# Kernel optimization log

Hardware: AMD Instinct MI355X
Metric: run time of the kernel (lower is better)

The kernel has to match this reference:

```python
import jax, jax.numpy as jnp
import numpy as np

# Llama-3-8B-like attention, prefill over B sequences of length S (flattened tokens)
D = 4096      # hidden_size
N = 32        # num query heads
K = 8         # num KV heads (GQA)
H = 128       # head_dim (== head_dim_original, already a multiple of 128 so no padding)
B = 4         # sequences in the ragged batch
S = 1024      # tokens per sequence
T = B * S     # total flattened tokens
ROPE_THETA = 10000.0


def _apply_rope(x, positions, head_dim, theta):
    # x: [T, n_heads, H]; positions: [T] int
    inv_freq = 1.0 / (theta ** (jnp.arange(0, head_dim, 2, dtype=jnp.float32) / head_dim))
    freqs = positions.astype(jnp.float32)[:, None] * inv_freq[None, :]  # [T, H/2]
    emb = jnp.concatenate([freqs, freqs], axis=-1)                       # [T, H]
    cos = jnp.cos(emb)[:, None, :].astype(x.dtype)
    sin = jnp.sin(emb)[:, None, :].astype(x.dtype)
    x1, x2 = jnp.split(x, 2, axis=-1)
    rotated = jnp.concatenate([-x2, x1], axis=-1)
    return x * cos + rotated * sin


def setup_inputs() -> dict:
    key = jax.random.key(0)
    ks = jax.random.split(key, 5)
    x = jax.random.normal(ks[0], (T, D), dtype=jnp.float32)
    # positions restart per sequence (ragged prefill metadata)
    input_positions = (jnp.arange(T, dtype=jnp.int32) % S)
    w_scale = 0.02
    Wq = jax.random.normal(ks[1], (D, N, H), dtype=jnp.float32) * w_scale
    Wk = jax.random.normal(ks[2], (D, K, H), dtype=jnp.float32) * w_scale
    Wv = jax.random.normal(ks[3], (D, K, H), dtype=jnp.float32) * w_scale
    Wo = jax.random.normal(ks[4], (N, H, D), dtype=jnp.float32) * w_scale
    return {"x": x, "input_positions": input_positions,
            "Wq": Wq, "Wk": Wk, "Wv": Wv, "Wo": Wo}


def reference(x, input_positions, Wq, Wk, Wv, Wo):
    # QKV projections (flattened tokens)
    q = jnp.einsum('td,dnh->tnh', x, Wq)   # [T, N, H]
    k = jnp.einsum('td,dkh->tkh', x, Wk)   # [T, K, H]
    v = jnp.einsum('td,dkh->tkh', x, Wv)   # [T, K, H]
    q = _apply_rope(q, input_positions, H, ROPE_THETA)
    k = _apply_rope(k, input_positions, H, ROPE_THETA)

    # Ragged causal attention: per-sequence causal SDPA with GQA head grouping.
    G = N // K  # query heads per KV head
    qb = q.reshape(B, S, K, G, H)
    kb = k.reshape(B, S, K, H)
    vb = v.reshape(B, S, K, H)
    scale = jnp.asarray(H, q.dtype) ** -0.5  # head_dim_original ** -0.5
    scores = jnp.einsum('bqkgh,bskh->bkgqs', qb, kb) * scale  # [B,K,G,S,S]
    causal = jnp.tril(jnp.ones((S, S), dtype=bool))
    scores = jnp.where(causal, scores, jnp.finfo(scores.dtype).min)
    probs = jax.nn.softmax(scores, axis=-1)
    out = jnp.einsum('bkgqs,bskh->bqkgh', probs, vb).reshape(T, N, H)

    # Output projection
    o = jnp.einsum('tnh,nhd->td', out, Wo)  # [T, D]
    return o
```

## Files before the change

kernel.cpp:

```cpp
#include <hip/hip_runtime.h>
#include <cstdint>


typedef unsigned short u16;
typedef short bf16x8 __attribute__((ext_vector_type(8)));
typedef float f32x4 __attribute__((ext_vector_type(4)));

#define L2E 1.44269504088896340736f

static __device__ __forceinline__ u16 f2bf(float f) {
  union { float f; unsigned u; } v; v.f = f;
  unsigned r = (v.u + 0x7fffu + ((v.u >> 16) & 1u)) >> 16;
  return (u16)r;
}
static __device__ __forceinline__ float bf2f(u16 h) {
  union { unsigned u; float f; } v; v.u = ((unsigned)h) << 16;
  return v.f;
}

typedef __attribute__((address_space(1))) const unsigned int gas_u32;
typedef __attribute__((address_space(3))) unsigned int las_u32;
static __device__ __forceinline__ void glds16(const void* g, const void* l) {
  __builtin_amdgcn_global_load_lds((gas_u32*)(uintptr_t)g,
                                   (las_u32*)(unsigned)(uintptr_t)l, 16, 0, 0);
}

__global__ __launch_bounds__(256) void cvt_kernel(const float4* __restrict__ in,
                                                  uint2* __restrict__ out, int n4) {
  int i = blockIdx.x * 256 + threadIdx.x;
  if (i < n4) {
    float4 v = in[i];
    uint2 r;
    r.x = (unsigned)f2bf(v.x) | ((unsigned)f2bf(v.y) << 16);
    r.y = (unsigned)f2bf(v.z) | ((unsigned)f2bf(v.w) << 16);
    out[i] = r;
  }
}

__global__ __launch_bounds__(256) void tcvt_kernel(const float* __restrict__ in,
                                                   u16* __restrict__ out, int R, int C) {
  __shared__ float tile[32][33];
  int tx = threadIdx.x, ty = threadIdx.y;
  int r0 = blockIdx.y * 32, c0 = blockIdx.x * 32;
#pragma unroll
  for (int j = 0; j < 4; ++j)
    tile[ty + j * 8][tx] = in[(size_t)(r0 + ty + j * 8) * C + c0 + tx];
  __syncthreads();
#pragma unroll
  for (int j = 0; j < 4; ++j)
    out[(size_t)(c0 + ty + j * 8) * R + r0 + tx] = f2bf(tile[tx][ty + j * 8]);
}

template <int BF16OUT>
__global__ __launch_bounds__(256, 2) void gemm_nt(const u16* __restrict__ A,
                                                  const u16* __restrict__ Bm,
                                                  void* __restrict__ Cp,
                                                  int M, int N, int Kd) {
  __shared__ u16 Al[128 * 64];
  __shared__ u16 Bl[128 * 64];
  const int tid = threadIdx.x;
  const int w = tid >> 6, lane = tid & 63;
  const int ln15 = lane & 15, quad = lane >> 4;
  const int wm = w & 1, wn = w >> 1;
  const int m0 = blockIdx.y * 128, n0 = blockIdx.x * 128;

  const int rA = w * 8 + (lane >> 3);
  const int cA = (((lane & 7) ^ (rA & 7)) << 3);
  const u16* aptr = A + (size_t)(m0 + rA) * Kd + cA;
  const u16* bptr = Bm + (size_t)(n0 + rA) * Kd + cA;

  f32x4 acc[4][4];
#pragma unroll
  for (int i = 0; i < 4; ++i)
#pragma unroll
    for (int j = 0; j < 4; ++j) acc[i][j] = f32x4{0.f, 0.f, 0.f, 0.f};

  for (int k0 = 0; k0 < Kd; k0 += 64) {
    __syncthreads();
#pragma unroll
    for (int q = 0; q < 4; ++q) {
      glds16(aptr + (size_t)q * 32 * Kd, &Al[(q * 32 + w * 8) * 64]);
      glds16(bptr + (size_t)q * 32 * Kd, &Bl[(q * 32 + w * 8) * 64]);
    }
    aptr += 64; bptr += 64;
    __syncthreads();
#pragma unroll
    for (int ks = 0; ks < 2; ++ks) {
      bf16x8 af[4], bfr[4];
#pragma unroll
      for (int t = 0; t < 4; ++t) {
        int ra = wm * 64 + t * 16 + ln15;
        int pa = (ks * 4 + quad) ^ (ra & 7);
        af[t] = *(const bf16x8*)&Al[ra * 64 + pa * 8];
        int rb = wn * 64 + t * 16 + ln15;
        int pb = (ks * 4 + quad) ^ (rb & 7);
        bfr[t] = *(const bf16x8*)&Bl[rb * 64 + pb * 8];
      }
#pragma unroll
      for (int mt = 0; mt < 4; ++mt)
#pragma unroll
        for (int nt = 0; nt < 4; ++nt)
          acc[mt][nt] =
              __builtin_amdgcn_mfma_f32_16x16x32_bf16(af[mt], bfr[nt], acc[mt][nt], 0, 0, 0);
    }
  }

#pragma unroll
  for (int mt = 0; mt < 4; ++mt) {
#pragma unroll
    for (int nt = 0; nt < 4; ++nt) {
      int row = m0 + wm * 64 + mt * 16 + quad * 4;
      int col = n0 + wn * 64 + nt * 16 + ln15;
#pragma unroll
      for (int r = 0; r < 4; ++r) {
        float v = acc[mt][nt][r];
        if (BF16OUT)
          ((u16*)Cp)[(size_t)(row + r) * N + col] = f2bf(v);
        else
          ((float*)Cp)[(size_t)(row + r) * N + col] = v;
      }
    }
  }
}

__global__ __launch_bounds__(256) void rope_kernel(u16* __restrict__ qkv,
                                                   const int* __restrict__ pos, int total) {
  int idx = blockIdx.x * 256 + threadIdx.x;
  if (idx >= total) return;
  int t = idx / 2560;
  int rem = idx - t * 2560;
  int head = rem >> 6;
  int i = rem & 63;
  float p = (float)pos[t];
  float inv = exp2f(-0.20751874963942190927f * (float)i);
  float f = p * inv;
  float s, c;
  sincosf(f, &s, &c);
  int colbase = (head < 32) ? head * 128 : (4096 + (head - 32) * 128);
  u16* base = qkv + (size_t)t * 6144 + colbase;
  float x1 = bf2f(base[i]), x2 = bf2f(base[i + 64]);
  float o1 = x1 * c - x2 * s;
  float o2 = x2 * c + x1 * s;
  if (head < 32) { o1 *= 0.08838834764831845f; o2 *= 0.08838834764831845f; }
  base[i] = f2bf(o1);
  base[i + 64] = f2bf(o2);
}

__global__ __launch_bounds__(256, 3) void attn_kernel(const u16* __restrict__ qkv,
                                                      u16* __restrict__ outp) {
  __shared__ u16 Klds[64 * 128];
  __shared__ u16 Vtlds[128 * 72];
  __shared__ u16 Plds[4 * 16 * 72];

  const int bx = blockIdx.x;
  const int qb = 15 - (bx & 15);
  const int n = (bx >> 4) & 31;
  const int b = bx >> 9;
  const int kh = n >> 2;

  const int tid = threadIdx.x;
  const int w = tid >> 6;
  const int lane = tid & 63;
  const int ln15 = lane & 15;
  const int quad = lane >> 4;

  const int ldq = 6144;
  const int seq0 = b << 10;
  const int q0 = seq0 + qb * 64;

  const u16* Qg = qkv + n * 128;
  const u16* Kg = qkv + 4096 + kh * 128;
  const u16* Vg = qkv + 5120 + kh * 128;

  bf16x8 qf[4];
  {
    const u16* qrow = Qg + (size_t)(q0 + w * 16 + ln15) * ldq + quad * 8;
#pragma unroll
    for (int ks = 0; ks < 4; ++ks) qf[ks] = *(const bf16x8*)(qrow + ks * 32);
  }

  f32x4 o[8];
#pragma unroll
  for (int i = 0; i < 8; ++i) o[i] = f32x4{0.f, 0.f, 0.f, 0.f};
  float m_r[4] = {-INFINITY, -INFINITY, -INFINITY, -INFINITY};
  float l_r[4] = {0.f, 0.f, 0.f, 0.f};

  const int krow = w * 4 + (lane >> 4);
  const int kcol = (((lane & 15) ^ (krow & 7)) << 3);

  const int vs0 = (lane & 31) * 2;
  const int vhb = w * 32 + (lane >> 5) * 16;

  for (int kt = 0; kt <= qb; ++kt) {
    __syncthreads();
    {
      const u16* kbase = Kg + (size_t)(seq0 + kt * 64 + krow) * ldq + kcol;
#pragma unroll
      for (int q = 0; q < 4; ++q)
        glds16(kbase + (size_t)q * 16 * ldq, &Klds[(q * 16 + w * 4) * 128]);
    }
    {
      const u16* v0 = Vg + (size_t)(seq0 + kt * 64 + vs0) * ldq + vhb;
      union { uint4 v[2]; u16 s[16]; } ra, rb;
      ra.v[0] = *(const uint4*)v0;
      ra.v[1] = *(const uint4*)(v0 + 8);
      rb.v[0] = *(const uint4*)(v0 + ldq);
      rb.v[1] = *(const uint4*)(v0 + ldq + 8);
#pragma unroll
      for (int j = 0; j < 16; ++j) {
        unsigned pk = (unsigned)ra.s[j] | ((unsigned)rb.s[j] << 16);
        *(unsigned*)&Vtlds[(vhb + j) * 72 + vs0] = pk;
      }
    }
    __syncthreads();

    f32x4 sfr[4];
#pragma unroll
    for (int c = 0; c < 4; ++c) {
      f32x4 acc = f32x4{0.f, 0.f, 0.f, 0.f};
#pragma unroll
      for (int ks = 0; ks < 4; ++ks) {
        int rr = c * 16 + ln15;
        int ph = (ks * 4 + quad) ^ (rr & 7);
        bf16x8 kf = *(const bf16x8*)&Klds[rr * 128 + ph * 8];
        acc = __builtin_amdgcn_mfma_f32_16x16x32_bf16(qf[ks], kf, acc, 0, 0, 0);
      }
      sfr[c] = acc;
    }

    if (kt == qb) {
#pragma unroll
      for (int c = 0; c < 4; ++c) {
        int col = c * 16 + ln15;
#pragma unroll
        for (int r = 0; r < 4; ++r)
          if (col > w * 16 + quad * 4 + r) sfr[c][r] = -INFINITY;
      }
    }

    float alpha[4];
#pragma unroll
    for (int r = 0; r < 4; ++r) {
      float mx = fmaxf(fmaxf(sfr[0][r], sfr[1][r]), fmaxf(sfr[2][r], sfr[3][r]));
      mx = fmaxf(mx, __shfl_xor(mx, 1));
      mx = fmaxf(mx, __shfl_xor(mx, 2));
      mx = fmaxf(mx, __shfl_xor(mx, 4));
      mx = fmaxf(mx, __shfl_xor(mx, 8));
      float mnew = fmaxf(m_r[r], mx);
      alpha[r] = exp2f((m_r[r] - mnew) * L2E);
      m_r[r] = mnew;
      float rs = 0.f;
#pragma unroll
      for (int c = 0; c < 4; ++c) {
        float pv = exp2f((sfr[c][r] - mnew) * L2E);
        sfr[c][r] = pv;
        rs += pv;
      }
      rs += __shfl_xor(rs, 1);
      rs += __shfl_xor(rs, 2);
      rs += __shfl_xor(rs, 4);
      rs += __shfl_xor(rs, 8);
      l_r[r] = alpha[r] * l_r[r] + rs;
    }

#pragma unroll
    for (int ht = 0; ht < 8; ++ht)
#pragma unroll
      for (int r = 0; r < 4; ++r) o[ht][r] *= alpha[r];

#pragma unroll
    for (int c = 0; c < 4; ++c)
#pragma unroll
      for (int r = 0; r < 4; ++r)
        Plds[w * 1152 + (quad * 4 + r) * 72 + c * 16 + ln15] = f2bf(sfr[c][r]);

    asm volatile("s_waitcnt lgkmcnt(0)" ::: "memory");

    bf16x8 pf[2];
#pragma unroll
    for (int ks = 0; ks < 2; ++ks)
      pf[ks] = *(const bf16x8*)&Plds[w * 1152 + ln15 * 72 + ks * 32 + quad * 8];
#pragma unroll
    for (int ht = 0; ht < 8; ++ht) {
#pragma unroll
      for (int ks = 0; ks < 2; ++ks) {
        bf16x8 vf = *(const bf16x8*)&Vtlds[(ht * 16 + ln15) * 72 + ks * 32 + quad * 8];
        o[ht] = __builtin_amdgcn_mfma_f32_16x16x32_bf16(pf[ks], vf, o[ht], 0, 0, 0);
      }
    }
  }

#pragma unroll
  for (int r = 0; r < 4; ++r) l_r[r] = 1.f / l_r[r];
#pragma unroll
  for (int ht = 0; ht < 8; ++ht)
#pragma unroll
    for (int r = 0; r < 4; ++r)
      outp[(size_t)(q0 + w * 16 + quad * 4 + r) * 4096 + n * 128 + ht * 16 + ln15] =
          f2bf(o[ht][r] * l_r[r]);
}

extern "C" void kernel_launch(void* const* d_in, const int* in_sizes, int n_in,
                              void* d_out, int out_size, void* d_ws, size_t ws_size,
                              hipStream_t stream) {
  const float* x = (const float*)d_in[0];
  const int* posi = (const int*)d_in[1];
  const float* Wq = (const float*)d_in[2];
  const float* Wk = (const float*)d_in[3];
  const float* Wv = (const float*)d_in[4];
  const float* Wo = (const float*)d_in[5];
  float* out = (float*)d_out;
  char* ws = (char*)d_ws;

  u16* xb = (u16*)(ws);
  u16* Wt = (u16*)(ws + 33554432);
  u16* WoT = (u16*)(ws + 83886080);
  u16* qkv = (u16*)(ws + 117440512);
  u16* attn = xb;

  cvt_kernel<<<16384, 256, 0, stream>>>((const float4*)x, (uint2*)xb, 4194304);
  tcvt_kernel<<<dim3(128, 128), dim3(32, 8), 0, stream>>>(Wq, Wt, 4096, 4096);
  tcvt_kernel<<<dim3(32, 128), dim3(32, 8), 0, stream>>>(Wk, Wt + (size_t)4096 * 4096, 4096, 1024);
  tcvt_kernel<<<dim3(32, 128), dim3(32, 8), 0, stream>>>(Wv, Wt + (size_t)5120 * 4096, 4096, 1024);
  tcvt_kernel<<<dim3(128, 128), dim3(32, 8), 0, stream>>>(Wo, WoT, 4096, 4096);

  gemm_nt<1><<<dim3(48, 32), 256, 0, stream>>>(xb, Wt, qkv, 4096, 6144, 4096);
  rope_kernel<<<40960, 256, 0, stream>>>(qkv, posi, 10485760);
  attn_kernel<<<2048, 256, 0, stream>>>(qkv, attn);
  gemm_nt<0><<<dim3(32, 32), 256, 0, stream>>>(attn, WoT, out, 4096, 4096, 4096);
}
```

Measured before the change: 793.0 us.

## Rewrite GEMMs as 256x256 8-wave double-buffered pipelined kernel with XCD swizzle

Replaces the 128x128 single-buffered 4-wave GEMM with a 256x256 tile, 512-thread kernel that double-buffers LDS and interleaves global-to-LDS prefetches with MFMA phases under explicit barriers, vmcnt waits and setprio. Block IDs are remapped so consecutive tiles land on the same XCD for L2 reuse. The goal is to hide load latency and raise arithmetic intensity in both projection GEMMs. In exchange it uses more registers and LDS per block and launches fewer blocks.

```diff
diff --git a/kernel.cpp b/kernel.cpp
--- a/kernel.cpp
+++ b/kernel.cpp
@@ -52,75 +52,120 @@
 }
 
 template <int BF16OUT>
-__global__ __launch_bounds__(256, 2) void gemm_nt(const u16* __restrict__ A,
-                                                  const u16* __restrict__ Bm,
-                                                  void* __restrict__ Cp,
-                                                  int M, int N, int Kd) {
-  __shared__ u16 Al[128 * 64];
-  __shared__ u16 Bl[128 * 64];
+__global__ __launch_bounds__(512, 2) void gemm_nt8(const u16* __restrict__ A,
+                                                   const u16* __restrict__ Bm,
+                                                   void* __restrict__ Cp,
+                                                   int M, int N, int Kd) {
+  __shared__ u16 Als[2][2][8192];
+  __shared__ u16 Bls[2][2][8192];
   const int tid = threadIdx.x;
   const int w = tid >> 6, lane = tid & 63;
   const int ln15 = lane & 15, quad = lane >> 4;
   const int wm = w & 1, wn = w >> 1;
-  const int m0 = blockIdx.y * 128, n0 = blockIdx.x * 128;
-
-  const int rA = w * 8 + (lane >> 3);
-  const int cA = (((lane & 7) ^ (rA & 7)) << 3);
-  const u16* aptr = A + (size_t)(m0 + rA) * Kd + cA;
-  const u16* bptr = Bm + (size_t)(n0 + rA) * Kd + cA;
-
-  f32x4 acc[4][4];
-#pragma unroll
-  for (int i = 0; i < 4; ++i)
+
+  const int nbm = M >> 8;
+  const int nwg = nbm * (N >> 8);
+  const int cpx = nwg >> 3;
+  const int bid = blockIdx.x;
+  const int swz = (bid & 7) * cpx + (bid >> 3);
+  const int bm = swz & (nbm - 1);
+  const int bn = swz / nbm;
+  const int m0 = bm << 8, n0 = bn << 8;
+
+  const int nt = Kd >> 6;
+
+  const int srow = lane >> 2;
+  const int schk = ((lane & 3) ^ ((lane >> 3) & 3)) << 3;
+  const u16* aSrc = A + (size_t)(m0 + w * 32 + srow) * Kd + schk;
+  const u16* bSrc = Bm + (size_t)(n0 + w * 32 + srow) * Kd + schk;
+  const int ldsb = w * 1024;
+
+  const int rswz = (quad ^ ((ln15 >> 1) & 3)) << 3;
+  const int aoff = (wm * 128 + ln15) * 32 + rswz;
+  const int boff = (wn * 64 + ln15) * 32 + rswz;
+
+  f32x4 acc[8][4];
+#pragma unroll
+  for (int i = 0; i < 8; ++i)
 #pragma unroll
     for (int j = 0; j < 4; ++j) acc[i][j] = f32x4{0.f, 0.f, 0.f, 0.f};
-
-  for (int k0 = 0; k0 < Kd; k0 += 64) {
-    __syncthreads();
-#pragma unroll
-    for (int q = 0; q < 4; ++q) {
-      glds16(aptr + (size_t)q * 32 * Kd, &Al[(q * 32 + w * 8) * 64]);
-      glds16(bptr + (size_t)q * 32 * Kd, &Bl[(q * 32 + w * 8) * 64]);
-    }
-    aptr += 64; bptr += 64;
-    __syncthreads();
-#pragma unroll
-    for (int ks = 0; ks < 2; ++ks) {
-      bf16x8 af[4], bfr[4];
-#pragma unroll
-      for (int t = 0; t < 4; ++t) {
-        int ra = wm * 64 + t * 16 + ln15;
-        int pa = (ks * 4 + quad) ^ (ra & 7);
-        af[t] = *(const bf16x8*)&Al[ra * 64 + pa * 8];
-        int rb = wn * 64 + t * 16 + ln15;
-        int pb = (ks * 4 + quad) ^ (rb & 7);
-        bfr[t] = *(const bf16x8*)&Bl[rb * 64 + pb * 8];
-      }
-#pragma unroll
-      for (int mt = 0; mt < 4; ++mt)
-#pragma unroll
-        for (int nt = 0; nt < 4; ++nt)
-          acc[mt][nt] =
-              __builtin_amdgcn_mfma_f32_16x16x32_bf16(af[mt], bfr[nt], acc[mt][nt], 0, 0, 0);
-    }
+  bf16x8 af[8];
+
+#define STA(kt, buf, ks)                                          \
+  do {                                                            \
+    int kc_ = (kt) < nt ? (kt) : nt - 1;                          \
+    const u16* s_ = aSrc + (size_t)kc_ * 64 + (ks) * 32;          \
+    glds16(s_, &Als[buf][ks][ldsb]);                              \
+    glds16(s_ + (size_t)16 * Kd, &Als[buf][ks][ldsb + 512]);      \
+  } while (0)
+#define STB(kt, buf, ks)                                          \
+  do {                                                            \
+    int kc_ = (kt) < nt ? (kt) : nt - 1;                          \
+    const u16* s_ = bSrc + (size_t)kc_ * 64 + (ks) * 32;          \
+    glds16(s_, &Bls[buf][ks][ldsb]);                              \
+    glds16(s_ + (size_t)16 * Kd, &Bls[buf][ks][ldsb + 512]);      \
+  } while (0)
+
+#define PHASE(buf, ks, nh, STAGE, VM)                                              \
+  do {                                                                             \
+    if ((nh) == 0) {                                                               \
+      _Pragma("unroll") for (int m_ = 0; m_ < 8; ++m_)                             \
+          af[m_] = *(const bf16x8*)&Als[buf][ks][aoff + m_ * 512];                 \
+    }                                                                              \
+    bf16x8 b0_ = *(const bf16x8*)&Bls[buf][ks][boff + (nh) * 1024];                \
+    bf16x8 b1_ = *(const bf16x8*)&Bls[buf][ks][boff + (nh) * 1024 + 512];          \
+    STAGE;                                                                         \
+    __builtin_amdgcn_s_barrier();                                                  \
+    __builtin_amdgcn_s_setprio(1);                                                 \
+    _Pragma("unroll") for (int m_ = 0; m_ < 8; ++m_) {                             \
+      acc[m_][2 * (nh)] =                                                          \
+          __builtin_amdgcn_mfma_f32_16x16x32_bf16(af[m_], b0_, acc[m_][2 * (nh)],  \
+                                                  0, 0, 0);                        \
+      acc[m_][2 * (nh) + 1] = __builtin_amdgcn_mfma_f32_16x16x32_bf16(             \
+          af[m_], b1_, acc[m_][2 * (nh) + 1], 0, 0, 0);                            \
+    }                                                                              \
+    __builtin_amdgcn_s_setprio(0);                                                 \
+    if (VM) asm volatile("s_waitcnt vmcnt(6)" ::: "memory");                       \
+    __builtin_amdgcn_s_barrier();                                                  \
+    __builtin_amdgcn_sched_barrier(0);                                             \
+  } while (0)
+
+  STA(0, 0, 0); STB(0, 0, 0); STA(0, 0, 1); STB(0, 0, 1);
+  STA(1, 1, 0); STB(1, 1, 0); STA(1, 1, 1);
+  asm volatile("s_waitcnt vmcnt(6)" ::: "memory");
+  __builtin_amdgcn_s_barrier();
+  __builtin_amdgcn_sched_barrier(0);
+
+  const int iters = nt >> 1;
+  for (int i = 0; i < iters; ++i) {
+    const int t = 2 * i;
+    PHASE(0, 0, 0, STB(t + 1, 1, 1), 0);
+    PHASE(0, 0, 1, STA(t + 2, 0, 0), 0);
+    PHASE(0, 1, 0, STB(t + 2, 0, 0), 0);
+    PHASE(0, 1, 1, STA(t + 2, 0, 1), 1);
+    PHASE(1, 0, 0, STB(t + 2, 0, 1), 0);
+    PHASE(1, 0, 1, STA(t + 3, 1, 0), 0);
+    PHASE(1, 1, 0, STB(t + 3, 1, 0), 0);
+    PHASE(1, 1, 1, STA(t + 3, 1, 1), 1);
   }
-
-#pragma unroll
-  for (int mt = 0; mt < 4; ++mt) {
-#pragma unroll
-    for (int nt = 0; nt < 4; ++nt) {
-      int row = m0 + wm * 64 + mt * 16 + quad * 4;
-      int col = n0 + wn * 64 + nt * 16 + ln15;
+#undef PHASE
+#undef STA
+#undef STB
+
+  const int crow = m0 + wm * 128 + quad * 4;
+  const int ccol = n0 + wn * 64 + ln15;
+#pragma unroll
+  for (int m = 0; m < 8; ++m)
+#pragma unroll
+    for (int j = 0; j < 4; ++j)
 #pragma unroll
       for (int r = 0; r < 4; ++r) {
-        float v = acc[mt][nt][r];
+        float v = acc[m][j][r];
         if (BF16OUT)
-          ((u16*)Cp)[(size_t)(row + r) * N + col] = f2bf(v);
+          ((u16*)Cp)[(size_t)(crow + m * 16 + r) * N + ccol + j * 16] = f2bf(v);
         else
-          ((float*)Cp)[(size_t)(row + r) * N + col] = v;
-      }
-    }
-  }
+          ((float*)Cp)[(size_t)(crow + m * 16 + r) * N + ccol + j * 16] = v;
+      }
 }
 
 __global__ __launch_bounds__(256) void rope_kernel(u16* __restrict__ qkv,
@@ -324,8 +369,8 @@
   tcvt_kernel<<<dim3(32, 128), dim3(32, 8), 0, stream>>>(Wv, Wt + (size_t)5120 * 4096, 4096, 1024);
   tcvt_kernel<<<dim3(128, 128), dim3(32, 8), 0, stream>>>(Wo, WoT, 4096, 4096);
 
-  gemm_nt<1><<<dim3(48, 32), 256, 0, stream>>>(xb, Wt, qkv, 4096, 6144, 4096);
+  gemm_nt8<1><<<dim3(384), 512, 0, stream>>>(xb, Wt, qkv, 4096, 6144, 4096);
   rope_kernel<<<40960, 256, 0, stream>>>(qkv, posi, 10485760);
   attn_kernel<<<2048, 256, 0, stream>>>(qkv, attn);
-  gemm_nt<0><<<dim3(32, 32), 256, 0, stream>>>(attn, WoT, out, 4096, 4096, 4096);
-}
+  gemm_nt8<0><<<dim3(256), 512, 0, stream>>>(attn, WoT, out, 4096, 4096, 4096);
+}
```

Result: no change. 782.5 us (-1.3%).
